# Kernel tuning notes

Measured on AMD Instinct MI355X. Metric: run time of the kernel, lower is better.

## Reference

```python
import jax, jax.numpy as jnp
import numpy as np

HIDDEN = 1024
B, S = 4, 2048

def setup_inputs() -> dict:
    key = jax.random.key(0)
    k1, k2 = jax.random.split(key)
    hidden_states = jax.random.normal(k1, (B, S, HIDDEN), dtype=jnp.float32)
    # torch nn.Linear weight layout: [out_features, in_features]
    W_proj = jax.random.normal(k2, (3 * HIDDEN, HIDDEN), dtype=jnp.float32) * (1.0 / np.sqrt(HIDDEN))
    b_proj = jnp.zeros((3 * HIDDEN,), dtype=jnp.float32)
    return {"hidden_states": hidden_states, "W_proj": W_proj, "b_proj": b_proj}

def reference(hidden_states, W_proj, b_proj):
    h = hidden_states.shape[-1]
    # fused QKV projection: y = x @ W^T + b
    qkv = jnp.einsum('bsh,oh->bso', hidden_states, W_proj) + b_proj
    q, k, v = jnp.split(qkv, 3, axis=-1)  # each [B,S,H]
    scale = 1.0 / jnp.sqrt(jnp.asarray(h, dtype=q.dtype))
    scores = jnp.einsum('bqh,bkh->bqk', q, k) * scale  # [B,S,S]
    attn = jax.nn.softmax(scores, axis=-1)
    out = jnp.einsum('bqk,bkh->bqh', attn, v)
    return out
```

## Files before the change

### kernel.cpp

```cpp
#include <hip/hip_runtime.h>
#include <stdint.h>

#define HIDDEN 1024
#define BATCH  4
#define SEQ    2048
#define TOKENS (BATCH * SEQ)
#define QKVD   (3 * HIDDEN)

typedef unsigned short u16;
typedef __attribute__((ext_vector_type(8))) short   short8;
typedef __attribute__((ext_vector_type(4))) float   floatx4;

__device__ __forceinline__ u16 f32_bf16_rne(float f) {
    unsigned int u = __float_as_uint(f);
    u += 0x7FFFu + ((u >> 16) & 1u);
    return (u16)(u >> 16);
}

#define BAR() asm volatile("s_waitcnt lgkmcnt(0)\n\ts_barrier" ::: "memory")

__global__ __launch_bounds__(256) void cvt_bf16_kernel(
        const float* __restrict__ src, u16* __restrict__ dst, int n4) {
    int i = blockIdx.x * 256 + threadIdx.x;
    if (i >= n4) return;
    float4 v = ((const float4*)src)[i];
    ushort4 o;
    o.x = f32_bf16_rne(v.x); o.y = f32_bf16_rne(v.y);
    o.z = f32_bf16_rne(v.z); o.w = f32_bf16_rne(v.w);
    ((ushort4*)dst)[i] = o;
}

struct Stage { uint4 a0, a1, b0, b1; };

template <int EPI>
__global__ __launch_bounds__(256, 3) void gemm_bt(
        const u16* __restrict__ A, const u16* __restrict__ B,
        void* __restrict__ Cv, const float* __restrict__ bias,
        int K, int lda, int ldb, int ldc,
        size_t sA, size_t sB, size_t sC, float scale) {
    __shared__ u16 As0[4096], As1[4096];
    __shared__ u16 Bs0[4096], Bs1[4096];

    const int t    = threadIdx.x;
    const int lane = t & 63;
    const int wid  = t >> 6;
    const int bm   = blockIdx.y * 128;
    const int bn   = blockIdx.x * 128;

    const u16* Ab = A + (size_t)blockIdx.z * sA;
    const u16* Bb = B + (size_t)blockIdx.z * sB;

    const int srow = lane >> 2;
    const int scol = ((lane & 3) ^ ((lane >> 3) & 3)) * 8;

    const int wm = (wid >> 1) * 64;
    const int wn = (wid & 1) * 64;
    const int fr = lane & 15;
    const int fc = lane >> 4;
    const int foff = fr * 32 + ((fc ^ ((fr >> 1) & 3)) * 8);

    const int c0 = wid * 2, c1 = wid * 2 + 1;
    const u16* gA0 = Ab + (size_t)(bm + c0 * 16 + srow) * lda + scol;
    const u16* gA1 = Ab + (size_t)(bm + c1 * 16 + srow) * lda + scol;
    const u16* gB0 = Bb + (size_t)(bn + c0 * 16 + srow) * ldb + scol;
    const u16* gB1 = Bb + (size_t)(bn + c1 * 16 + srow) * ldb + scol;

    const int nk = K >> 5;

    auto ldst = [&](int kt) -> Stage {
        Stage s;
        const int off = kt << 5;
        s.a0 = *(const uint4*)(gA0 + off);
        s.a1 = *(const uint4*)(gA1 + off);
        s.b0 = *(const uint4*)(gB0 + off);
        s.b1 = *(const uint4*)(gB1 + off);
        return s;
    };
    auto wst = [&](u16* As_, u16* Bs_, const Stage& s) {
        *(uint4*)&As_[c0 * 512 + lane * 8] = s.a0;
        *(uint4*)&As_[c1 * 512 + lane * 8] = s.a1;
        *(uint4*)&Bs_[c0 * 512 + lane * 8] = s.b0;
        *(uint4*)&Bs_[c1 * 512 + lane * 8] = s.b1;
    };

    floatx4 acc[4][4];
#pragma unroll
    for (int i = 0; i < 4; i++)
#pragma unroll
        for (int j = 0; j < 4; j++) acc[i][j] = (floatx4){0.f, 0.f, 0.f, 0.f};

    auto compute = [&](const u16* As_, const u16* Bs_) {
        short8 bfr[4];
#pragma unroll
        for (int ni = 0; ni < 4; ni++)
            bfr[ni] = *(const short8*)&Bs_[((wn >> 4) + ni) * 512 + foff];
#pragma unroll
        for (int mi = 0; mi < 4; mi++) {
            short8 a = *(const short8*)&As_[((wm >> 4) + mi) * 512 + foff];
#pragma unroll
            for (int ni = 0; ni < 4; ni++)
                acc[mi][ni] = __builtin_amdgcn_mfma_f32_16x16x32_bf16(
                    a, bfr[ni], acc[mi][ni], 0, 0, 0);
        }
    };

    Stage ra = ldst(0);
    Stage rb = ldst(nk > 1 ? 1 : 0);
    wst(As0, Bs0, ra);
    BAR();

    for (int kt = 0; kt < nk; kt += 2) {
        ra = ldst(kt + 2 < nk ? kt + 2 : nk - 1);
        compute(As0, Bs0);
        wst(As1, Bs1, rb);
        BAR();
        rb = ldst(kt + 3 < nk ? kt + 3 : nk - 1);
        compute(As1, Bs1);
        wst(As0, Bs0, ra);
        BAR();
    }

    const int crow0 = bm + wm + (lane >> 4) * 4;
    const int ccol0 = bn + wn + fr;
    const size_t coff = (size_t)blockIdx.z * sC;

    if (EPI == 0) {
        u16* C = (u16*)Cv;
        float bv[4];
#pragma unroll
        for (int ni = 0; ni < 4; ni++) bv[ni] = bias[ccol0 + ni * 16];
#pragma unroll
        for (int mi = 0; mi < 4; mi++)
#pragma unroll
            for (int ni = 0; ni < 4; ni++)
#pragma unroll
                for (int r = 0; r < 4; r++)
                    C[coff + (size_t)(crow0 + mi * 16 + r) * ldc + (ccol0 + ni * 16)] =
                        f32_bf16_rne(acc[mi][ni][r] + bv[ni]);
    } else {
        float* C = (float*)Cv;
#pragma unroll
        for (int mi = 0; mi < 4; mi++)
#pragma unroll
            for (int ni = 0; ni < 4; ni++)
#pragma unroll
                for (int r = 0; r < 4; r++) {
                    float v = acc[mi][ni][r];
                    if (EPI == 1) v *= scale;
                    C[coff + (size_t)(crow0 + mi * 16 + r) * ldc + (ccol0 + ni * 16)] = v;
                }
    }
}

__global__ __launch_bounds__(256) void softmax_kernel(
        const float* __restrict__ S, u16* __restrict__ P) {
    __shared__ float redm[4];
    __shared__ float reds[4];
    const size_t base = (size_t)blockIdx.x * SEQ;
    const int t = threadIdx.x, lane = t & 63, wid = t >> 6;
    const float4* src = (const float4*)(S + base);
    float4 a = src[t], b = src[t + 256];

    float m = fmaxf(fmaxf(fmaxf(a.x, a.y), fmaxf(a.z, a.w)),
                    fmaxf(fmaxf(b.x, b.y), fmaxf(b.z, b.w)));
#pragma unroll
    for (int off = 32; off; off >>= 1) m = fmaxf(m, __shfl_xor(m, off, 64));
    if (lane == 0) redm[wid] = m;
    __syncthreads();
    m = fmaxf(fmaxf(redm[0], redm[1]), fmaxf(redm[2], redm[3]));

    float e[8];
    e[0] = __expf(a.x - m); e[1] = __expf(a.y - m);
    e[2] = __expf(a.z - m); e[3] = __expf(a.w - m);
    e[4] = __expf(b.x - m); e[5] = __expf(b.y - m);
    e[6] = __expf(b.z - m); e[7] = __expf(b.w - m);
    float s = e[0] + e[1] + e[2] + e[3] + e[4] + e[5] + e[6] + e[7];
#pragma unroll
    for (int off = 32; off; off >>= 1) s += __shfl_xor(s, off, 64);
    if (lane == 0) reds[wid] = s;
    __syncthreads();
    s = reds[0] + reds[1] + reds[2] + reds[3];
    const float r = 1.f / s;

    ushort4* dst = (ushort4*)(P + base);
    ushort4 o0, o1;
    o0.x = f32_bf16_rne(e[0] * r); o0.y = f32_bf16_rne(e[1] * r);
    o0.z = f32_bf16_rne(e[2] * r); o0.w = f32_bf16_rne(e[3] * r);
    o1.x = f32_bf16_rne(e[4] * r); o1.y = f32_bf16_rne(e[5] * r);
    o1.z = f32_bf16_rne(e[6] * r); o1.w = f32_bf16_rne(e[7] * r);
    dst[t] = o0;
    dst[t + 256] = o1;
}

__global__ __launch_bounds__(256) void transposeV_kernel(
        const u16* __restrict__ qkv, u16* __restrict__ Vt) {
    __shared__ u16 tile[64][66];
    const int b = blockIdx.z;
    const int s0 = blockIdx.x * 64, h0 = blockIdx.y * 64;
    const int t = threadIdx.x;
    const int c = t & 63, r4 = t >> 6;
#pragma unroll
    for (int i = 0; i < 16; i++) {
        int sl = i * 4 + r4;
        tile[sl][c] = qkv[(size_t)(b * SEQ + s0 + sl) * QKVD + 2 * HIDDEN + h0 + c];
    }
    __syncthreads();
#pragma unroll
    for (int i = 0; i < 16; i++) {
        int hl = i * 4 + r4;
        Vt[(size_t)(b * HIDDEN + h0 + hl) * SEQ + s0 + c] = tile[c][hl];
    }
}

extern "C" void kernel_launch(void* const* d_in, const int* in_sizes, int n_in,
                              void* d_out, int out_size, void* d_ws, size_t ws_size,
                              hipStream_t stream) {
    const float* x    = (const float*)d_in[0];
    const float* W    = (const float*)d_in[1];
    const float* bias = (const float*)d_in[2];
    float* out = (float*)d_out;

    u16* Xb  = (u16*)d_ws;
    u16* Wb  = Xb + (size_t)TOKENS * HIDDEN;
    u16* qkv = Wb + (size_t)QKVD * HIDDEN;
    float* scores = (float*)(qkv + (size_t)TOKENS * QKVD);
    u16* P  = (u16*)(scores + (size_t)BATCH * SEQ * SEQ);
    u16* Vt = P + (size_t)BATCH * SEQ * SEQ;

    cvt_bf16_kernel<<<TOKENS * HIDDEN / 4 / 256, 256, 0, stream>>>(x, Xb, TOKENS * HIDDEN / 4);
    cvt_bf16_kernel<<<QKVD * HIDDEN / 4 / 256, 256, 0, stream>>>(W, Wb, QKVD * HIDDEN / 4);

    gemm_bt<0><<<dim3(QKVD / 128, TOKENS / 128, 1), 256, 0, stream>>>(
        Xb, Wb, qkv, bias, HIDDEN, HIDDEN, HIDDEN, QKVD, 0, 0, 0, 1.f);

    gemm_bt<1><<<dim3(SEQ / 128, SEQ / 128, BATCH), 256, 0, stream>>>(
        qkv, qkv + HIDDEN, scores, nullptr, HIDDEN, QKVD, QKVD, SEQ,
        (size_t)SEQ * QKVD, (size_t)SEQ * QKVD, (size_t)SEQ * SEQ, 0.03125f);

    softmax_kernel<<<BATCH * SEQ, 256, 0, stream>>>(scores, P);

    transposeV_kernel<<<dim3(SEQ / 64, HIDDEN / 64, BATCH), 256, 0, stream>>>(qkv, Vt);

    gemm_bt<2><<<dim3(HIDDEN / 128, SEQ / 128, BATCH), 256, 0, stream>>>(
        P, Vt, out, nullptr, SEQ, SEQ, SEQ, HIDDEN,
        (size_t)SEQ * SEQ, (size_t)HIDDEN * SEQ, (size_t)SEQ * HIDDEN, 1.f);
}
```

Baseline: 275.7 us.

## Rewrite GEMM mainloop with direct global-to-LDS loads and 128x256 tiles

The bf16 GEMM now uses global_load_lds to move tiles straight into shared memory instead of staging them through registers. The block tile grows to 128x256 with 512 threads (8 waves), and each K step covers 64 with a double-buffered LDS ring. Synchronisation uses s_waitcnt vmcnt with barriers, and MFMA groups run at raised priority via setprio. This targets register-staging overhead and LDS write cost, in exchange for more LDS per block, fewer blocks in the grid, and delicate vmcnt accounting that could break correctness.

```diff
diff --git a/kernel.cpp b/kernel.cpp
--- a/kernel.cpp
+++ b/kernel.cpp
@@ -17,7 +17,14 @@
     return (u16)(u >> 16);
 }
 
-#define BAR() asm volatile("s_waitcnt lgkmcnt(0)\n\ts_barrier" ::: "memory")
+__device__ __forceinline__ void gl16(const u16* g, u16* l) {
+    __builtin_amdgcn_global_load_lds(
+        (const __attribute__((address_space(1))) void*)g,
+        (__attribute__((address_space(3))) void*)l, 16, 0, 0);
+}
+
+#define SYNC3() do { __builtin_amdgcn_sched_barrier(0); \
+    asm volatile("s_waitcnt vmcnt(3)\n\ts_barrier" ::: "memory"); } while (0)
 
 __global__ __launch_bounds__(256) void cvt_bf16_kernel(
         const float* __restrict__ src, u16* __restrict__ dst, int n4) {
@@ -30,58 +37,39 @@
     ((ushort4*)dst)[i] = o;
 }
 
-struct Stage { uint4 a0, a1, b0, b1; };
-
 template <int EPI>
-__global__ __launch_bounds__(256, 3) void gemm_bt(
+__global__ __launch_bounds__(512, 2) void gemm_bt(
         const u16* __restrict__ A, const u16* __restrict__ B,
         void* __restrict__ Cv, const float* __restrict__ bias,
         int K, int lda, int ldb, int ldc,
         size_t sA, size_t sB, size_t sC, float scale) {
-    __shared__ u16 As0[4096], As1[4096];
-    __shared__ u16 Bs0[4096], Bs1[4096];
+    __shared__ __align__(16) u16 lds[2][2][(128 + 256) * 32];
 
     const int t    = threadIdx.x;
     const int lane = t & 63;
     const int wid  = t >> 6;
+    const int wr   = wid >> 2;
+    const int wc   = wid & 3;
     const int bm   = blockIdx.y * 128;
-    const int bn   = blockIdx.x * 128;
+    const int bn   = blockIdx.x * 256;
 
     const u16* Ab = A + (size_t)blockIdx.z * sA;
     const u16* Bb = B + (size_t)blockIdx.z * sB;
 
-    const int srow = lane >> 2;
-    const int scol = ((lane & 3) ^ ((lane >> 3) & 3)) * 8;
-
-    const int wm = (wid >> 1) * 64;
-    const int wn = (wid & 1) * 64;
+    const int rA   = t >> 2;
+    const int slA  = (t & 3) ^ ((rA >> 1) & 3);
+    const u16* gA  = Ab + (size_t)(bm + rA) * lda + slA * 8;
+    const int rB   = t >> 2;
+    const int slB  = (t & 3) ^ ((rB >> 1) & 3);
+    const u16* gB0 = Bb + (size_t)(bn + rB) * ldb + slB * 8;
+    const u16* gB1 = gB0 + (size_t)128 * ldb;
+
     const int fr = lane & 15;
-    const int fc = lane >> 4;
-    const int foff = fr * 32 + ((fc ^ ((fr >> 1) & 3)) * 8);
-
-    const int c0 = wid * 2, c1 = wid * 2 + 1;
-    const u16* gA0 = Ab + (size_t)(bm + c0 * 16 + srow) * lda + scol;
-    const u16* gA1 = Ab + (size_t)(bm + c1 * 16 + srow) * lda + scol;
-    const u16* gB0 = Bb + (size_t)(bn + c0 * 16 + srow) * ldb + scol;
-    const u16* gB1 = Bb + (size_t)(bn + c1 * 16 + srow) * ldb + scol;
-
-    const int nk = K >> 5;
-
-    auto ldst = [&](int kt) -> Stage {
-        Stage s;
-        const int off = kt << 5;
-        s.a0 = *(const uint4*)(gA0 + off);
-        s.a1 = *(const uint4*)(gA1 + off);
-        s.b0 = *(const uint4*)(gB0 + off);
-        s.b1 = *(const uint4*)(gB1 + off);
-        return s;
-    };
-    auto wst = [&](u16* As_, u16* Bs_, const Stage& s) {
-        *(uint4*)&As_[c0 * 512 + lane * 8] = s.a0;
-        *(uint4*)&As_[c1 * 512 + lane * 8] = s.a1;
-        *(uint4*)&Bs_[c0 * 512 + lane * 8] = s.b0;
-        *(uint4*)&Bs_[c1 * 512 + lane * 8] = s.b1;
-    };
+    const int kc = lane >> 4;
+    const int sw = (fr >> 1) & 3;
+    const int fo = (kc ^ sw) << 4;
+    const int aoffB = (wr * 64 + fr) * 64 + fo;
+    const int boffB = (wc * 64 + fr) * 64 + fo;
 
     floatx4 acc[4][4];
 #pragma unroll
@@ -89,39 +77,81 @@
 #pragma unroll
         for (int j = 0; j < 4; j++) acc[i][j] = (floatx4){0.f, 0.f, 0.f, 0.f};
 
-    auto compute = [&](const u16* As_, const u16* Bs_) {
-        short8 bfr[4];
-#pragma unroll
-        for (int ni = 0; ni < 4; ni++)
-            bfr[ni] = *(const short8*)&Bs_[((wn >> 4) + ni) * 512 + foff];
-#pragma unroll
-        for (int mi = 0; mi < 4; mi++) {
-            short8 a = *(const short8*)&As_[((wm >> 4) + mi) * 512 + foff];
-#pragma unroll
-            for (int ni = 0; ni < 4; ni++)
-                acc[mi][ni] = __builtin_amdgcn_mfma_f32_16x16x32_bf16(
-                    a, bfr[ni], acc[mi][ni], 0, 0, 0);
-        }
-    };
-
-    Stage ra = ldst(0);
-    Stage rb = ldst(nk > 1 ? 1 : 0);
-    wst(As0, Bs0, ra);
-    BAR();
-
+    short8 bfr0, bfr1, bfr2, bfr3, va0, va1;
+
+#define LDB4(BASE) \
+    bfr0 = *(const short8*)((BASE) + boffB);        \
+    bfr1 = *(const short8*)((BASE) + boffB + 1024); \
+    bfr2 = *(const short8*)((BASE) + boffB + 2048); \
+    bfr3 = *(const short8*)((BASE) + boffB + 3072);
+
+#define MFMA2(MI, A0, A1) \
+    __builtin_amdgcn_s_setprio(1); \
+    acc[MI][0]     = __builtin_amdgcn_mfma_f32_16x16x32_bf16(A0, bfr0, acc[MI][0], 0, 0, 0); \
+    acc[MI][1]     = __builtin_amdgcn_mfma_f32_16x16x32_bf16(A0, bfr1, acc[MI][1], 0, 0, 0); \
+    acc[MI][2]     = __builtin_amdgcn_mfma_f32_16x16x32_bf16(A0, bfr2, acc[MI][2], 0, 0, 0); \
+    acc[MI][3]     = __builtin_amdgcn_mfma_f32_16x16x32_bf16(A0, bfr3, acc[MI][3], 0, 0, 0); \
+    acc[(MI)+1][0] = __builtin_amdgcn_mfma_f32_16x16x32_bf16(A1, bfr0, acc[(MI)+1][0], 0, 0, 0); \
+    acc[(MI)+1][1] = __builtin_amdgcn_mfma_f32_16x16x32_bf16(A1, bfr1, acc[(MI)+1][1], 0, 0, 0); \
+    acc[(MI)+1][2] = __builtin_amdgcn_mfma_f32_16x16x32_bf16(A1, bfr2, acc[(MI)+1][2], 0, 0, 0); \
+    acc[(MI)+1][3] = __builtin_amdgcn_mfma_f32_16x16x32_bf16(A1, bfr3, acc[(MI)+1][3], 0, 0, 0); \
+    __builtin_amdgcn_s_setprio(0);
+
+#define ITER(BUF, SBUF, SCOL) { \
+    const char* As0_ = (const char*)&lds[BUF][0][0]; \
+    const char* Bs0_ = As0_ + 8192; \
+    const char* As1_ = (const char*)&lds[BUF][1][0]; \
+    const char* Bs1_ = As1_ + 8192; \
+     \
+    gl16(gA + (SCOL),       (u16*)((char*)&lds[SBUF][0][0]    + wid * 1024)); \
+    LDB4(Bs0_); \
+    va0 = *(const short8*)(As0_ + aoffB); \
+    va1 = *(const short8*)(As0_ + aoffB + 1024); \
+    MFMA2(0, va0, va1); \
+     \
+    gl16(gB0 + (SCOL),      (u16*)((char*)&lds[SBUF][0][4096] + wid * 1024)); \
+    gl16(gB1 + (SCOL),      (u16*)((char*)&lds[SBUF][0][8192] + wid * 1024)); \
+    va0 = *(const short8*)(As0_ + aoffB + 2048); \
+    va1 = *(const short8*)(As0_ + aoffB + 3072); \
+    MFMA2(2, va0, va1); \
+    SYNC3(); \
+     \
+    gl16(gA + (SCOL) + 32,  (u16*)((char*)&lds[SBUF][1][0]    + wid * 1024)); \
+    LDB4(Bs1_); \
+    va0 = *(const short8*)(As1_ + aoffB); \
+    va1 = *(const short8*)(As1_ + aoffB + 1024); \
+    MFMA2(0, va0, va1); \
+     \
+    gl16(gB0 + (SCOL) + 32, (u16*)((char*)&lds[SBUF][1][4096] + wid * 1024)); \
+    gl16(gB1 + (SCOL) + 32, (u16*)((char*)&lds[SBUF][1][8192] + wid * 1024)); \
+    va0 = *(const short8*)(As1_ + aoffB + 2048); \
+    va1 = *(const short8*)(As1_ + aoffB + 3072); \
+    MFMA2(2, va0, va1); \
+    SYNC3(); }
+
+    gl16(gA,       (u16*)((char*)&lds[0][0][0]    + wid * 1024));
+    gl16(gB0,      (u16*)((char*)&lds[0][0][4096] + wid * 1024));
+    gl16(gB1,      (u16*)((char*)&lds[0][0][8192] + wid * 1024));
+    gl16(gA + 32,  (u16*)((char*)&lds[0][1][0]    + wid * 1024));
+    gl16(gB0 + 32, (u16*)((char*)&lds[0][1][4096] + wid * 1024));
+    gl16(gB1 + 32, (u16*)((char*)&lds[0][1][8192] + wid * 1024));
+    SYNC3();
+
+    const int nk = K >> 6;
     for (int kt = 0; kt < nk; kt += 2) {
-        ra = ldst(kt + 2 < nk ? kt + 2 : nk - 1);
-        compute(As0, Bs0);
-        wst(As1, Bs1, rb);
-        BAR();
-        rb = ldst(kt + 3 < nk ? kt + 3 : nk - 1);
-        compute(As1, Bs1);
-        wst(As0, Bs0, ra);
-        BAR();
-    }
-
-    const int crow0 = bm + wm + (lane >> 4) * 4;
-    const int ccol0 = bn + wn + fr;
+        const int c1 = (kt + 1) * 64;
+        const int c2 = (kt + 2 < nk ? (kt + 2) : (nk - 1)) * 64;
+        ITER(0, 1, c1)
+        ITER(1, 0, c2)
+    }
+    asm volatile("s_waitcnt vmcnt(0)" ::: "memory");
+
+#undef ITER
+#undef MFMA2
+#undef LDB4
+
+    const int crow0 = bm + wr * 64 + kc * 4;
+    const int ccol0 = bn + wc * 64 + fr;
     const size_t coff = (size_t)blockIdx.z * sC;
 
     if (EPI == 0) {
@@ -230,10 +260,10 @@
     cvt_bf16_kernel<<<TOKENS * HIDDEN / 4 / 256, 256, 0, stream>>>(x, Xb, TOKENS * HIDDEN / 4);
     cvt_bf16_kernel<<<QKVD * HIDDEN / 4 / 256, 256, 0, stream>>>(W, Wb, QKVD * HIDDEN / 4);
 
-    gemm_bt<0><<<dim3(QKVD / 128, TOKENS / 128, 1), 256, 0, stream>>>(
+    gemm_bt<0><<<dim3(QKVD / 256, TOKENS / 128, 1), 512, 0, stream>>>(
         Xb, Wb, qkv, bias, HIDDEN, HIDDEN, HIDDEN, QKVD, 0, 0, 0, 1.f);
 
-    gemm_bt<1><<<dim3(SEQ / 128, SEQ / 128, BATCH), 256, 0, stream>>>(
+    gemm_bt<1><<<dim3(SEQ / 256, SEQ / 128, BATCH), 512, 0, stream>>>(
         qkv, qkv + HIDDEN, scores, nullptr, HIDDEN, QKVD, QKVD, SEQ,
         (size_t)SEQ * QKVD, (size_t)SEQ * QKVD, (size_t)SEQ * SEQ, 0.03125f);
 
@@ -241,7 +271,7 @@
 
     transposeV_kernel<<<dim3(SEQ / 64, HIDDEN / 64, BATCH), 256, 0, stream>>>(qkv, Vt);
 
-    gemm_bt<2><<<dim3(HIDDEN / 128, SEQ / 128, BATCH), 256, 0, stream>>>(
+    gemm_bt<2><<<dim3(HIDDEN / 256, SEQ / 128, BATCH), 512, 0, stream>>>(
         P, Vt, out, nullptr, SEQ, SEQ, SEQ, HIDDEN,
         (size_t)SEQ * SEQ, (size_t)HIDDEN * SEQ, (size_t)SEQ * HIDDEN, 1.f);
 }
```

Measured after the change: 268.0 us. 1.03x faster.

## Rewrite GEMM with 256x256 tiles, direct global-to-LDS loads and 4-stage pipeline

Applied to the files above, without the earlier changes.

The GEMM moves from 128x128 tiles with 256 threads to 256x256 tiles with 512 threads. Operands are staged through a 4-buffer LDS ring using global_load_lds, which skips the register round-trip. Waits use vmcnt-based barriers and s_setprio around MFMA bursts. The two fp32-to-bf16 conversion launches are also merged into one. The aim is more data reuse per tile and better overlap of memory and compute, at the cost of 128KB of LDS, higher register pressure (128 accumulator floats per lane) and fewer blocks for the smaller GEMMs.

```diff
diff --git a/kernel.cpp b/kernel.cpp
--- a/kernel.cpp
+++ b/kernel.cpp
@@ -17,111 +17,132 @@
     return (u16)(u >> 16);
 }
 
-#define BAR() asm volatile("s_waitcnt lgkmcnt(0)\n\ts_barrier" ::: "memory")
-
-__global__ __launch_bounds__(256) void cvt_bf16_kernel(
-        const float* __restrict__ src, u16* __restrict__ dst, int n4) {
+__device__ __forceinline__ void gl16(const u16* g, u16* l) {
+    __builtin_amdgcn_global_load_lds(
+        (const __attribute__((address_space(1))) void*)g,
+        (__attribute__((address_space(3))) void*)l, 16, 0, 0);
+}
+
+#define SYNC8() do { __builtin_amdgcn_sched_barrier(0); \
+    asm volatile("s_waitcnt vmcnt(8)\n\ts_barrier" ::: "memory"); } while (0)
+
+__global__ __launch_bounds__(256) void cvt2_bf16_kernel(
+        const float* __restrict__ sa, const float* __restrict__ sb,
+        u16* __restrict__ da, u16* __restrict__ db, int n4a, int n4tot) {
     int i = blockIdx.x * 256 + threadIdx.x;
-    if (i >= n4) return;
-    float4 v = ((const float4*)src)[i];
+    if (i >= n4tot) return;
+    float4 v;
+    if (i < n4a) v = ((const float4*)sa)[i];
+    else         v = ((const float4*)sb)[i - n4a];
     ushort4 o;
     o.x = f32_bf16_rne(v.x); o.y = f32_bf16_rne(v.y);
     o.z = f32_bf16_rne(v.z); o.w = f32_bf16_rne(v.w);
-    ((ushort4*)dst)[i] = o;
-}
-
-struct Stage { uint4 a0, a1, b0, b1; };
+    if (i < n4a) ((ushort4*)da)[i] = o;
+    else         ((ushort4*)db)[i - n4a] = o;
+}
 
 template <int EPI>
-__global__ __launch_bounds__(256, 3) void gemm_bt(
+__global__ __launch_bounds__(512, 2) void gemm_bt(
         const u16* __restrict__ A, const u16* __restrict__ B,
         void* __restrict__ Cv, const float* __restrict__ bias,
         int K, int lda, int ldb, int ldc,
         size_t sA, size_t sB, size_t sC, float scale) {
-    __shared__ u16 As0[4096], As1[4096];
-    __shared__ u16 Bs0[4096], Bs1[4096];
+    __shared__ __align__(16) u16 lds[4][16384];
 
     const int t    = threadIdx.x;
     const int lane = t & 63;
     const int wid  = t >> 6;
-    const int bm   = blockIdx.y * 128;
-    const int bn   = blockIdx.x * 128;
+    const int wr   = wid >> 2;
+    const int wc   = wid & 3;
+    const int bm   = blockIdx.y * 256;
+    const int bn   = blockIdx.x * 256;
 
     const u16* Ab = A + (size_t)blockIdx.z * sA;
     const u16* Bb = B + (size_t)blockIdx.z * sB;
 
-    const int srow = lane >> 2;
-    const int scol = ((lane & 3) ^ ((lane >> 3) & 3)) * 8;
-
-    const int wm = (wid >> 1) * 64;
-    const int wn = (wid & 1) * 64;
+    const int r0 = t >> 2;
+    const int sl = (t & 3) ^ ((r0 >> 1) & 3);
+    const u16* gA0 = Ab + (size_t)(bm + r0) * lda + sl * 8;
+    const u16* gA1 = gA0 + (size_t)128 * lda;
+    const u16* gB0 = Bb + (size_t)(bn + r0) * ldb + sl * 8;
+    const u16* gB1 = gB0 + (size_t)128 * ldb;
+
     const int fr = lane & 15;
-    const int fc = lane >> 4;
-    const int foff = fr * 32 + ((fc ^ ((fr >> 1) & 3)) * 8);
-
-    const int c0 = wid * 2, c1 = wid * 2 + 1;
-    const u16* gA0 = Ab + (size_t)(bm + c0 * 16 + srow) * lda + scol;
-    const u16* gA1 = Ab + (size_t)(bm + c1 * 16 + srow) * lda + scol;
-    const u16* gB0 = Bb + (size_t)(bn + c0 * 16 + srow) * ldb + scol;
-    const u16* gB1 = Bb + (size_t)(bn + c1 * 16 + srow) * ldb + scol;
+    const int kc = lane >> 4;
+    const int fo = ((kc ^ ((fr >> 1) & 3)) << 4);
+    const int abyte = (wr * 128 + fr) * 64 + fo;
+    const int bbyte = 16384 + (wc * 64 + fr) * 64 + fo;
+
+    floatx4 acc[8][4];
+#pragma unroll
+    for (int i = 0; i < 8; i++)
+#pragma unroll
+        for (int j = 0; j < 4; j++) acc[i][j] = (floatx4){0.f, 0.f, 0.f, 0.f};
+
+#define STAGE_A(p, scol) \
+    gl16(gA0 + (scol), &lds[p][wid * 512]); \
+    gl16(gA1 + (scol), &lds[p][4096 + wid * 512]);
+#define STAGE_B(p, scol) \
+    gl16(gB0 + (scol), &lds[p][8192  + wid * 512]); \
+    gl16(gB1 + (scol), &lds[p][12288 + wid * 512]);
+
+#define MF4(MI, AV) \
+    acc[MI][0] = __builtin_amdgcn_mfma_f32_16x16x32_bf16(AV, b0, acc[MI][0], 0, 0, 0); \
+    acc[MI][1] = __builtin_amdgcn_mfma_f32_16x16x32_bf16(AV, b1, acc[MI][1], 0, 0, 0); \
+    acc[MI][2] = __builtin_amdgcn_mfma_f32_16x16x32_bf16(AV, b2, acc[MI][2], 0, 0, 0); \
+    acc[MI][3] = __builtin_amdgcn_mfma_f32_16x16x32_bf16(AV, b3, acc[MI][3], 0, 0, 0);
+
+#define STEP(q, p, scol) { \
+    const char* base = (const char*)&lds[q][0]; \
+     \
+    STAGE_A(p, scol); \
+    short8 b0 = *(const short8*)(base + bbyte); \
+    short8 b1 = *(const short8*)(base + bbyte + 1024); \
+    short8 b2 = *(const short8*)(base + bbyte + 2048); \
+    short8 b3 = *(const short8*)(base + bbyte + 3072); \
+    short8 a0 = *(const short8*)(base + abyte); \
+    short8 a1 = *(const short8*)(base + abyte + 1024); \
+    short8 a2 = *(const short8*)(base + abyte + 2048); \
+    short8 a3 = *(const short8*)(base + abyte + 3072); \
+    __builtin_amdgcn_s_setprio(1); \
+    MF4(0, a0) MF4(1, a1) MF4(2, a2) MF4(3, a3) \
+    __builtin_amdgcn_s_setprio(0); \
+     \
+    STAGE_B(p, scol); \
+    a0 = *(const short8*)(base + abyte + 4096); \
+    a1 = *(const short8*)(base + abyte + 5120); \
+    a2 = *(const short8*)(base + abyte + 6144); \
+    a3 = *(const short8*)(base + abyte + 7168); \
+    __builtin_amdgcn_s_setprio(1); \
+    MF4(4, a0) MF4(5, a1) MF4(6, a2) MF4(7, a3) \
+    __builtin_amdgcn_s_setprio(0); \
+    SYNC8(); }
+
+    STAGE_A(0, 0)  STAGE_B(0, 0)
+    STAGE_A(1, 32) STAGE_B(1, 32)
+    STAGE_A(2, 64) STAGE_B(2, 64)
+    SYNC8();
 
     const int nk = K >> 5;
-
-    auto ldst = [&](int kt) -> Stage {
-        Stage s;
-        const int off = kt << 5;
-        s.a0 = *(const uint4*)(gA0 + off);
-        s.a1 = *(const uint4*)(gA1 + off);
-        s.b0 = *(const uint4*)(gB0 + off);
-        s.b1 = *(const uint4*)(gB1 + off);
-        return s;
-    };
-    auto wst = [&](u16* As_, u16* Bs_, const Stage& s) {
-        *(uint4*)&As_[c0 * 512 + lane * 8] = s.a0;
-        *(uint4*)&As_[c1 * 512 + lane * 8] = s.a1;
-        *(uint4*)&Bs_[c0 * 512 + lane * 8] = s.b0;
-        *(uint4*)&Bs_[c1 * 512 + lane * 8] = s.b1;
-    };
-
-    floatx4 acc[4][4];
-#pragma unroll
-    for (int i = 0; i < 4; i++)
-#pragma unroll
-        for (int j = 0; j < 4; j++) acc[i][j] = (floatx4){0.f, 0.f, 0.f, 0.f};
-
-    auto compute = [&](const u16* As_, const u16* Bs_) {
-        short8 bfr[4];
-#pragma unroll
-        for (int ni = 0; ni < 4; ni++)
-            bfr[ni] = *(const short8*)&Bs_[((wn >> 4) + ni) * 512 + foff];
-#pragma unroll
-        for (int mi = 0; mi < 4; mi++) {
-            short8 a = *(const short8*)&As_[((wm >> 4) + mi) * 512 + foff];
-#pragma unroll
-            for (int ni = 0; ni < 4; ni++)
-                acc[mi][ni] = __builtin_amdgcn_mfma_f32_16x16x32_bf16(
-                    a, bfr[ni], acc[mi][ni], 0, 0, 0);
-        }
-    };
-
-    Stage ra = ldst(0);
-    Stage rb = ldst(nk > 1 ? 1 : 0);
-    wst(As0, Bs0, ra);
-    BAR();
-
-    for (int kt = 0; kt < nk; kt += 2) {
-        ra = ldst(kt + 2 < nk ? kt + 2 : nk - 1);
-        compute(As0, Bs0);
-        wst(As1, Bs1, rb);
-        BAR();
-        rb = ldst(kt + 3 < nk ? kt + 3 : nk - 1);
-        compute(As1, Bs1);
-        wst(As0, Bs0, ra);
-        BAR();
-    }
-
-    const int crow0 = bm + wm + (lane >> 4) * 4;
-    const int ccol0 = bn + wn + fr;
+    for (int kt = 0; kt < nk; kt += 4) {
+        const int s0 = (kt + 3 < nk ? kt + 3 : nk - 1) << 5;
+        const int s1 = (kt + 4 < nk ? kt + 4 : nk - 1) << 5;
+        const int s2 = (kt + 5 < nk ? kt + 5 : nk - 1) << 5;
+        const int s3 = (kt + 6 < nk ? kt + 6 : nk - 1) << 5;
+        STEP(0, 3, s0)
+        STEP(1, 0, s1)
+        STEP(2, 1, s2)
+        STEP(3, 2, s3)
+    }
+    asm volatile("s_waitcnt vmcnt(0)" ::: "memory");
+
+#undef STEP
+#undef MF4
+#undef STAGE_A
+#undef STAGE_B
+
+    const int crow0 = bm + wr * 128 + kc * 4;
+    const int ccol0 = bn + wc * 64 + fr;
     const size_t coff = (size_t)blockIdx.z * sC;
 
     if (EPI == 0) {
@@ -130,7 +151,7 @@
 #pragma unroll
         for (int ni = 0; ni < 4; ni++) bv[ni] = bias[ccol0 + ni * 16];
 #pragma unroll
-        for (int mi = 0; mi < 4; mi++)
+        for (int mi = 0; mi < 8; mi++)
 #pragma unroll
             for (int ni = 0; ni < 4; ni++)
 #pragma unroll
@@ -140,7 +161,7 @@
     } else {
         float* C = (float*)Cv;
 #pragma unroll
-        for (int mi = 0; mi < 4; mi++)
+        for (int mi = 0; mi < 8; mi++)
 #pragma unroll
             for (int ni = 0; ni < 4; ni++)
 #pragma unroll
@@ -227,13 +248,17 @@
     u16* P  = (u16*)(scores + (size_t)BATCH * SEQ * SEQ);
     u16* Vt = P + (size_t)BATCH * SEQ * SEQ;
 
-    cvt_bf16_kernel<<<TOKENS * HIDDEN / 4 / 256, 256, 0, stream>>>(x, Xb, TOKENS * HIDDEN / 4);
-    cvt_bf16_kernel<<<QKVD * HIDDEN / 4 / 256, 256, 0, stream>>>(W, Wb, QKVD * HIDDEN / 4);
-
-    gemm_bt<0><<<dim3(QKVD / 128, TOKENS / 128, 1), 256, 0, stream>>>(
+    {
+        const int n4a = TOKENS * HIDDEN / 4;
+        const int n4b = QKVD * HIDDEN / 4;
+        const int n4t = n4a + n4b;
+        cvt2_bf16_kernel<<<(n4t + 255) / 256, 256, 0, stream>>>(x, W, Xb, Wb, n4a, n4t);
+    }
+
+    gemm_bt<0><<<dim3(QKVD / 256, TOKENS / 256, 1), 512, 0, stream>>>(
         Xb, Wb, qkv, bias, HIDDEN, HIDDEN, HIDDEN, QKVD, 0, 0, 0, 1.f);
 
-    gemm_bt<1><<<dim3(SEQ / 128, SEQ / 128, BATCH), 256, 0, stream>>>(
+    gemm_bt<1><<<dim3(SEQ / 256, SEQ / 256, BATCH), 512, 0, stream>>>(
         qkv, qkv + HIDDEN, scores, nullptr, HIDDEN, QKVD, QKVD, SEQ,
         (size_t)SEQ * QKVD, (size_t)SEQ * QKVD, (size_t)SEQ * SEQ, 0.03125f);
 
@@ -241,7 +266,7 @@
 
     transposeV_kernel<<<dim3(SEQ / 64, HIDDEN / 64, BATCH), 256, 0, stream>>>(qkv, Vt);
 
-    gemm_bt<2><<<dim3(HIDDEN / 128, SEQ / 128, BATCH), 256, 0, stream>>>(
+    gemm_bt<2><<<dim3(HIDDEN / 256, SEQ / 256, BATCH), 512, 0, stream>>>(
         P, Vt, out, nullptr, SEQ, SEQ, SEQ, HIDDEN,
         (size_t)SEQ * SEQ, (size_t)HIDDEN * SEQ, (size_t)SEQ * HIDDEN, 1.f);
 }
```

Result: no change. 280.8 us (+1.9%).

## Stage GEMM tiles via direct global-to-LDS loads and merge small kernels

Applied to the files above, without the earlier changes.

The GEMM main loop now issues global_load_lds intrinsics that copy tiles straight into LDS, with a new swizzled layout, so tiles no longer pass through registers. This is meant to cut VGPR staging and LDS write instructions. The two bf16 conversion kernels are merged into one launch, and the V transpose is folded into the softmax kernel as extra blocks, removing two launches. The risk is that the loads are no longer prefetched before compute in the same way: loads are issued and then waited on at the barrier, so latency hiding may be weaker.

```diff
diff --git a/kernel.cpp b/kernel.cpp
--- a/kernel.cpp
+++ b/kernel.cpp
@@ -17,110 +17,105 @@
     return (u16)(u >> 16);
 }
 
-#define BAR() asm volatile("s_waitcnt lgkmcnt(0)\n\ts_barrier" ::: "memory")
-
-__global__ __launch_bounds__(256) void cvt_bf16_kernel(
-        const float* __restrict__ src, u16* __restrict__ dst, int n4) {
+__device__ __forceinline__ void gl16(const u16* g, u16* l) {
+    __builtin_amdgcn_global_load_lds(
+        (const __attribute__((address_space(1))) void*)g,
+        (__attribute__((address_space(3))) void*)l, 16, 0, 0);
+}
+
+__global__ __launch_bounds__(256) void cvt2_bf16_kernel(
+        const float* __restrict__ sa, const float* __restrict__ sb,
+        u16* __restrict__ da, u16* __restrict__ db, int n4a, int n4tot) {
     int i = blockIdx.x * 256 + threadIdx.x;
-    if (i >= n4) return;
-    float4 v = ((const float4*)src)[i];
+    if (i >= n4tot) return;
+    float4 v;
+    if (i < n4a) v = ((const float4*)sa)[i];
+    else         v = ((const float4*)sb)[i - n4a];
     ushort4 o;
     o.x = f32_bf16_rne(v.x); o.y = f32_bf16_rne(v.y);
     o.z = f32_bf16_rne(v.z); o.w = f32_bf16_rne(v.w);
-    ((ushort4*)dst)[i] = o;
-}
-
-struct Stage { uint4 a0, a1, b0, b1; };
+    if (i < n4a) ((ushort4*)da)[i] = o;
+    else         ((ushort4*)db)[i - n4a] = o;
+}
 
 template <int EPI>
-__global__ __launch_bounds__(256, 3) void gemm_bt(
+__global__ __launch_bounds__(256, 3) void gemm_m97(
         const u16* __restrict__ A, const u16* __restrict__ B,
         void* __restrict__ Cv, const float* __restrict__ bias,
         int K, int lda, int ldb, int ldc,
         size_t sA, size_t sB, size_t sC, float scale) {
-    __shared__ u16 As0[4096], As1[4096];
-    __shared__ u16 Bs0[4096], Bs1[4096];
+    __shared__ __align__(16) char lds[2][16384];
 
     const int t    = threadIdx.x;
     const int lane = t & 63;
     const int wid  = t >> 6;
+    const int wm   = (wid >> 1) * 64;
+    const int wn   = (wid & 1) * 64;
     const int bm   = blockIdx.y * 128;
     const int bn   = blockIdx.x * 128;
 
     const u16* Ab = A + (size_t)blockIdx.z * sA;
     const u16* Bb = B + (size_t)blockIdx.z * sB;
 
-    const int srow = lane >> 2;
-    const int scol = ((lane & 3) ^ ((lane >> 3) & 3)) * 8;
-
-    const int wm = (wid >> 1) * 64;
-    const int wn = (wid & 1) * 64;
-    const int fr = lane & 15;
-    const int fc = lane >> 4;
-    const int foff = fr * 32 + ((fc ^ ((fr >> 1) & 3)) * 8);
-
-    const int c0 = wid * 2, c1 = wid * 2 + 1;
-    const u16* gA0 = Ab + (size_t)(bm + c0 * 16 + srow) * lda + scol;
-    const u16* gA1 = Ab + (size_t)(bm + c1 * 16 + srow) * lda + scol;
-    const u16* gB0 = Bb + (size_t)(bn + c0 * 16 + srow) * ldb + scol;
-    const u16* gB1 = Bb + (size_t)(bn + c1 * 16 + srow) * ldb + scol;
-
-    const int nk = K >> 5;
-
-    auto ldst = [&](int kt) -> Stage {
-        Stage s;
-        const int off = kt << 5;
-        s.a0 = *(const uint4*)(gA0 + off);
-        s.a1 = *(const uint4*)(gA1 + off);
-        s.b0 = *(const uint4*)(gB0 + off);
-        s.b1 = *(const uint4*)(gB1 + off);
-        return s;
+    const int r0 = t >> 2;
+    const int sl = (t & 3) ^ ((r0 >> 1) & 3);
+    const u16* gA0 = Ab + (size_t)(bm + r0) * lda + sl * 8;
+    const u16* gA1 = gA0 + (size_t)64 * lda;
+    const u16* gB0 = Bb + (size_t)(bn + r0) * ldb + sl * 8;
+    const u16* gB1 = gB0 + (size_t)64 * ldb;
+
+    const int fr   = lane & 15;
+    const int kc   = lane >> 4;
+    const int fo   = (kc ^ ((fr >> 1) & 3)) << 4;
+    const int aoff = (wm + fr) * 64 + fo;
+    const int boff = 8192 + (wn + fr) * 64 + fo;
+
+    floatx4 acc[4][4];
+#pragma unroll
+    for (int i = 0; i < 4; i++)
+#pragma unroll
+        for (int j = 0; j < 4; j++) acc[i][j] = (floatx4){0.f, 0.f, 0.f, 0.f};
+
+    auto stage = [&](int q, int kcol) {
+        char* d = &lds[q][0] + t * 16;
+        gl16(gA0 + kcol, (u16*)d);
+        gl16(gA1 + kcol, (u16*)(d + 4096));
+        gl16(gB0 + kcol, (u16*)(d + 8192));
+        gl16(gB1 + kcol, (u16*)(d + 12288));
     };
-    auto wst = [&](u16* As_, u16* Bs_, const Stage& s) {
-        *(uint4*)&As_[c0 * 512 + lane * 8] = s.a0;
-        *(uint4*)&As_[c1 * 512 + lane * 8] = s.a1;
-        *(uint4*)&Bs_[c0 * 512 + lane * 8] = s.b0;
-        *(uint4*)&Bs_[c1 * 512 + lane * 8] = s.b1;
-    };
-
-    floatx4 acc[4][4];
-#pragma unroll
-    for (int i = 0; i < 4; i++)
-#pragma unroll
-        for (int j = 0; j < 4; j++) acc[i][j] = (floatx4){0.f, 0.f, 0.f, 0.f};
-
-    auto compute = [&](const u16* As_, const u16* Bs_) {
-        short8 bfr[4];
-#pragma unroll
-        for (int ni = 0; ni < 4; ni++)
-            bfr[ni] = *(const short8*)&Bs_[((wn >> 4) + ni) * 512 + foff];
+    auto comp = [&](const char* bp) {
+        short8 a0 = *(const short8*)(bp + aoff);
+        short8 a1 = *(const short8*)(bp + aoff + 1024);
+        short8 a2 = *(const short8*)(bp + aoff + 2048);
+        short8 a3 = *(const short8*)(bp + aoff + 3072);
+        short8 b0 = *(const short8*)(bp + boff);
+        short8 b1 = *(const short8*)(bp + boff + 1024);
+        short8 b2 = *(const short8*)(bp + boff + 2048);
+        short8 b3 = *(const short8*)(bp + boff + 3072);
 #pragma unroll
         for (int mi = 0; mi < 4; mi++) {
-            short8 a = *(const short8*)&As_[((wm >> 4) + mi) * 512 + foff];
-#pragma unroll
-            for (int ni = 0; ni < 4; ni++)
-                acc[mi][ni] = __builtin_amdgcn_mfma_f32_16x16x32_bf16(
-                    a, bfr[ni], acc[mi][ni], 0, 0, 0);
+            short8 av = (mi == 0) ? a0 : (mi == 1) ? a1 : (mi == 2) ? a2 : a3;
+            acc[mi][0] = __builtin_amdgcn_mfma_f32_16x16x32_bf16(av, b0, acc[mi][0], 0, 0, 0);
+            acc[mi][1] = __builtin_amdgcn_mfma_f32_16x16x32_bf16(av, b1, acc[mi][1], 0, 0, 0);
+            acc[mi][2] = __builtin_amdgcn_mfma_f32_16x16x32_bf16(av, b2, acc[mi][2], 0, 0, 0);
+            acc[mi][3] = __builtin_amdgcn_mfma_f32_16x16x32_bf16(av, b3, acc[mi][3], 0, 0, 0);
         }
     };
 
-    Stage ra = ldst(0);
-    Stage rb = ldst(nk > 1 ? 1 : 0);
-    wst(As0, Bs0, ra);
-    BAR();
-
+    stage(0, 0);
+    __syncthreads();
+
+    const int nk = K >> 5;
     for (int kt = 0; kt < nk; kt += 2) {
-        ra = ldst(kt + 2 < nk ? kt + 2 : nk - 1);
-        compute(As0, Bs0);
-        wst(As1, Bs1, rb);
-        BAR();
-        rb = ldst(kt + 3 < nk ? kt + 3 : nk - 1);
-        compute(As1, Bs1);
-        wst(As0, Bs0, ra);
-        BAR();
-    }
-
-    const int crow0 = bm + wm + (lane >> 4) * 4;
+        stage(1, (kt + 1) << 5);
+        comp(lds[0]);
+        __syncthreads();
+        stage(0, (kt + 2 < nk ? kt + 2 : nk - 1) << 5);
+        comp(lds[1]);
+        __syncthreads();
+    }
+
+    const int crow0 = bm + wm + kc * 4;
     const int ccol0 = bn + wn + fr;
     const size_t coff = (size_t)blockIdx.z * sC;
 
@@ -152,63 +147,66 @@
     }
 }
 
-__global__ __launch_bounds__(256) void softmax_kernel(
-        const float* __restrict__ S, u16* __restrict__ P) {
+__global__ __launch_bounds__(256) void softmax_tr_kernel(
+        const float* __restrict__ S, u16* __restrict__ P,
+        const u16* __restrict__ qkv, u16* __restrict__ Vt) {
     __shared__ float redm[4];
     __shared__ float reds[4];
-    const size_t base = (size_t)blockIdx.x * SEQ;
-    const int t = threadIdx.x, lane = t & 63, wid = t >> 6;
-    const float4* src = (const float4*)(S + base);
-    float4 a = src[t], b = src[t + 256];
-
-    float m = fmaxf(fmaxf(fmaxf(a.x, a.y), fmaxf(a.z, a.w)),
-                    fmaxf(fmaxf(b.x, b.y), fmaxf(b.z, b.w)));
-#pragma unroll
-    for (int off = 32; off; off >>= 1) m = fmaxf(m, __shfl_xor(m, off, 64));
-    if (lane == 0) redm[wid] = m;
-    __syncthreads();
-    m = fmaxf(fmaxf(redm[0], redm[1]), fmaxf(redm[2], redm[3]));
-
-    float e[8];
-    e[0] = __expf(a.x - m); e[1] = __expf(a.y - m);
-    e[2] = __expf(a.z - m); e[3] = __expf(a.w - m);
-    e[4] = __expf(b.x - m); e[5] = __expf(b.y - m);
-    e[6] = __expf(b.z - m); e[7] = __expf(b.w - m);
-    float s = e[0] + e[1] + e[2] + e[3] + e[4] + e[5] + e[6] + e[7];
-#pragma unroll
-    for (int off = 32; off; off >>= 1) s += __shfl_xor(s, off, 64);
-    if (lane == 0) reds[wid] = s;
-    __syncthreads();
-    s = reds[0] + reds[1] + reds[2] + reds[3];
-    const float r = 1.f / s;
-
-    ushort4* dst = (ushort4*)(P + base);
-    ushort4 o0, o1;
-    o0.x = f32_bf16_rne(e[0] * r); o0.y = f32_bf16_rne(e[1] * r);
-    o0.z = f32_bf16_rne(e[2] * r); o0.w = f32_bf16_rne(e[3] * r);
-    o1.x = f32_bf16_rne(e[4] * r); o1.y = f32_bf16_rne(e[5] * r);
-    o1.z = f32_bf16_rne(e[6] * r); o1.w = f32_bf16_rne(e[7] * r);
-    dst[t] = o0;
-    dst[t + 256] = o1;
-}
-
-__global__ __launch_bounds__(256) void transposeV_kernel(
-        const u16* __restrict__ qkv, u16* __restrict__ Vt) {
     __shared__ u16 tile[64][66];
-    const int b = blockIdx.z;
-    const int s0 = blockIdx.x * 64, h0 = blockIdx.y * 64;
     const int t = threadIdx.x;
-    const int c = t & 63, r4 = t >> 6;
-#pragma unroll
-    for (int i = 0; i < 16; i++) {
-        int sl = i * 4 + r4;
-        tile[sl][c] = qkv[(size_t)(b * SEQ + s0 + sl) * QKVD + 2 * HIDDEN + h0 + c];
-    }
-    __syncthreads();
-#pragma unroll
-    for (int i = 0; i < 16; i++) {
-        int hl = i * 4 + r4;
-        Vt[(size_t)(b * HIDDEN + h0 + hl) * SEQ + s0 + c] = tile[c][hl];
+
+    if ((int)blockIdx.x < TOKENS) {
+        const size_t base = (size_t)blockIdx.x * SEQ;
+        const int lane = t & 63, wid = t >> 6;
+        const float4* src = (const float4*)(S + base);
+        float4 a = src[t], b = src[t + 256];
+
+        float m = fmaxf(fmaxf(fmaxf(a.x, a.y), fmaxf(a.z, a.w)),
+                        fmaxf(fmaxf(b.x, b.y), fmaxf(b.z, b.w)));
+#pragma unroll
+        for (int off = 32; off; off >>= 1) m = fmaxf(m, __shfl_xor(m, off, 64));
+        if (lane == 0) redm[wid] = m;
+        __syncthreads();
+        m = fmaxf(fmaxf(redm[0], redm[1]), fmaxf(redm[2], redm[3]));
+
+        float e[8];
+        e[0] = __expf(a.x - m); e[1] = __expf(a.y - m);
+        e[2] = __expf(a.z - m); e[3] = __expf(a.w - m);
+        e[4] = __expf(b.x - m); e[5] = __expf(b.y - m);
+        e[6] = __expf(b.z - m); e[7] = __expf(b.w - m);
+        float s = e[0] + e[1] + e[2] + e[3] + e[4] + e[5] + e[6] + e[7];
+#pragma unroll
+        for (int off = 32; off; off >>= 1) s += __shfl_xor(s, off, 64);
+        if (lane == 0) reds[wid] = s;
+        __syncthreads();
+        s = reds[0] + reds[1] + reds[2] + reds[3];
+        const float r = 1.f / s;
+
+        ushort4* dst = (ushort4*)(P + base);
+        ushort4 o0, o1;
+        o0.x = f32_bf16_rne(e[0] * r); o0.y = f32_bf16_rne(e[1] * r);
+        o0.z = f32_bf16_rne(e[2] * r); o0.w = f32_bf16_rne(e[3] * r);
+        o1.x = f32_bf16_rne(e[4] * r); o1.y = f32_bf16_rne(e[5] * r);
+        o1.z = f32_bf16_rne(e[6] * r); o1.w = f32_bf16_rne(e[7] * r);
+        dst[t] = o0;
+        dst[t + 256] = o1;
+    } else {
+        const int bx = blockIdx.x - TOKENS;
+        const int b  = bx >> 9;
+        const int s0 = (bx & 31) * 64;
+        const int h0 = ((bx >> 5) & 15) * 64;
+        const int c = t & 63, r4 = t >> 6;
+#pragma unroll
+        for (int i = 0; i < 16; i++) {
+            int sl = i * 4 + r4;
+            tile[sl][c] = qkv[(size_t)(b * SEQ + s0 + sl) * QKVD + 2 * HIDDEN + h0 + c];
+        }
+        __syncthreads();
+#pragma unroll
+        for (int i = 0; i < 16; i++) {
+            int hl = i * 4 + r4;
+            Vt[(size_t)(b * HIDDEN + h0 + hl) * SEQ + s0 + c] = tile[c][hl];
+        }
     }
 }
 
@@ -227,21 +225,23 @@
     u16* P  = (u16*)(scores + (size_t)BATCH * SEQ * SEQ);
     u16* Vt = P + (size_t)BATCH * SEQ * SEQ;
 
-    cvt_bf16_kernel<<<TOKENS * HIDDEN / 4 / 256, 256, 0, stream>>>(x, Xb, TOKENS * HIDDEN / 4);
-    cvt_bf16_kernel<<<QKVD * HIDDEN / 4 / 256, 256, 0, stream>>>(W, Wb, QKVD * HIDDEN / 4);
-
-    gemm_bt<0><<<dim3(QKVD / 128, TOKENS / 128, 1), 256, 0, stream>>>(
+    {
+        const int n4a = TOKENS * HIDDEN / 4;
+        const int n4b = QKVD * HIDDEN / 4;
+        const int n4t = n4a + n4b;
+        cvt2_bf16_kernel<<<(n4t + 255) / 256, 256, 0, stream>>>(x, W, Xb, Wb, n4a, n4t);
+    }
+
+    gemm_m97<0><<<dim3(QKVD / 128, TOKENS / 128, 1), 256, 0, stream>>>(
         Xb, Wb, qkv, bias, HIDDEN, HIDDEN, HIDDEN, QKVD, 0, 0, 0, 1.f);
 
-    gemm_bt<1><<<dim3(SEQ / 128, SEQ / 128, BATCH), 256, 0, stream>>>(
+    gemm_m97<1><<<dim3(SEQ / 128, SEQ / 128, BATCH), 256, 0, stream>>>(
         qkv, qkv + HIDDEN, scores, nullptr, HIDDEN, QKVD, QKVD, SEQ,
         (size_t)SEQ * QKVD, (size_t)SEQ * QKVD, (size_t)SEQ * SEQ, 0.03125f);
 
-    softmax_kernel<<<BATCH * SEQ, 256, 0, stream>>>(scores, P);
-
-    transposeV_kernel<<<dim3(SEQ / 64, HIDDEN / 64, BATCH), 256, 0, stream>>>(qkv, Vt);
-
-    gemm_bt<2><<<dim3(HIDDEN / 128, SEQ / 128, BATCH), 256, 0, stream>>>(
+    softmax_tr_kernel<<<TOKENS + 2048, 256, 0, stream>>>(scores, P, qkv, Vt);
+
+    gemm_m97<2><<<dim3(HIDDEN / 128, SEQ / 128, BATCH), 256, 0, stream>>>(
         P, Vt, out, nullptr, SEQ, SEQ, SEQ, HIDDEN,
         (size_t)SEQ * SEQ, (size_t)HIDDEN * SEQ, (size_t)SEQ * HIDDEN, 1.f);
 }
```

After: 267.8 us. 2.9% less time.
